# Kernel optimization log

Measured on AMD Instinct MI355X. Metric: run time of the kernel, lower is better.

Reference implementation:

```python
import jax, jax.numpy as jnp
import numpy as np

D_MODEL = 1024
NUM_HEADS = 16
D_K = D_MODEL // NUM_HEADS
NEG = -1000000000.0


def setup_inputs() -> dict:
    key = jax.random.key(0)
    ks = jax.random.split(key, 9)
    B, S, D = 2, 2048, D_MODEL
    scale = 1.0 / np.sqrt(D)
    return {
        "query": jax.random.normal(ks[0], (B, S, D), jnp.float32),
        "key": jax.random.normal(ks[1], (B, S, D), jnp.float32),
        "value": jax.random.normal(ks[2], (B, S, D), jnp.float32),
        "mask": jax.random.randint(ks[3], (B, S, S), 0, 2, jnp.int32),
        # torch nn.Linear stores weight as (out_features, in_features); y = x @ W.T
        "W_q": jax.random.normal(ks[4], (D, D), jnp.float32) * scale,
        "W_k": jax.random.normal(ks[5], (D, D), jnp.float32) * scale,
        "W_v": jax.random.normal(ks[6], (D, D), jnp.float32) * scale,
        "W_o": jax.random.normal(ks[7], (D, D), jnp.float32) * scale,
        "b_o": jax.random.normal(ks[8], (D,), jnp.float32) * 0.01,
    }


def reference(query, key, value, mask, W_q, W_k, W_v, W_o, b_o):
    B, S, D = query.shape
    H, dk = NUM_HEADS, D_K
    # projections (torch Linear: x @ W.T), then split heads -> [B, H, S, dk]
    def split_heads(x, W):
        return jnp.einsum('bsd,ed->bse', x, W).reshape(B, S, H, dk).transpose(0, 2, 1, 3)
    Q = split_heads(query, W_q)
    K = split_heads(key, W_k)
    V = split_heads(value, W_v)
    scores = jnp.einsum('bhqd,bhkd->bhqk', Q, K) / jnp.sqrt(jnp.float32(dk))
    scores = jnp.where(mask[:, None, :, :] == 0, NEG, scores)
    attn = jax.nn.softmax(scores, axis=-1)  # dropout inactive in eval mode
    out = jnp.einsum('bhqk,bhkd->bhqd', attn, V)  # [B, H, S, dk]
    out = out.transpose(0, 2, 1, 3).reshape(B, S, D)
    return jnp.einsum('bsd,ed->bse', out, W_o) + b_o
```

## Files before the change

kernel.cpp:

```cpp
#include <hip/hip_runtime.h>
#include <hip/hip_bf16.h>
#include <stdint.h>

typedef __attribute__((ext_vector_type(4))) float f32x4;
typedef __attribute__((ext_vector_type(8))) short bf16x8;
typedef __attribute__((ext_vector_type(4))) unsigned short us4;
typedef unsigned short ushort_t;
typedef unsigned long long u64;

#define LOG2E 1.44269504088896340f
#define NEGB  -1.0e9f

__device__ __forceinline__ unsigned short f2bf(float x){
  union { float f; uint32_t u; } v; v.f = x;
  uint32_t u = v.u + 0x7fffu + ((v.u >> 16) & 1u);
  return (unsigned short)(u >> 16);
}

__device__ __forceinline__ void gld16(const void* g, void* l){
  __builtin_amdgcn_global_load_lds(
      (const __attribute__((address_space(1))) unsigned int*)g,
      (__attribute__((address_space(3))) unsigned int*)l, 16, 0, 0);
}

__global__ void prep_all(const float4* __restrict__ q, const float4* __restrict__ k,
                         const float4* __restrict__ v, const float4* __restrict__ wq,
                         const float4* __restrict__ wk, const float4* __restrict__ wv,
                         const float4* __restrict__ wo, ushort_t* __restrict__ dst){
  int i = blockIdx.x * 256 + threadIdx.x;
  const float4* src; int base;
  if      (i < 1048576){ src = q;  base = 0; }
  else if (i < 2097152){ src = k;  base = 1048576; }
  else if (i < 3145728){ src = v;  base = 2097152; }
  else if (i < 3407872){ src = wq; base = 3145728; }
  else if (i < 3670016){ src = wk; base = 3407872; }
  else if (i < 3932160){ src = wv; base = 3670016; }
  else                 { src = wo; base = 3932160; }
  float4 f = src[i - base];
  us4 o; o.x = f2bf(f.x); o.y = f2bf(f.y); o.z = f2bf(f.z); o.w = f2bf(f.w);
  ((us4*)dst)[i] = o;
}

__global__ void gemm_qkv(const ushort_t* __restrict__ qb, const ushort_t* __restrict__ kb,
                         const ushort_t* __restrict__ vb, const ushort_t* __restrict__ wqb,
                         const ushort_t* __restrict__ wkb, const ushort_t* __restrict__ wvb,
                         ushort_t* __restrict__ Qh, ushort_t* __restrict__ Kh,
                         ushort_t* __restrict__ Vt, float qscale,
                         const int4* __restrict__ mask, u64* __restrict__ mb){
  __shared__ ushort_t smem[16384];
#define AsQ(c) (smem + (c)*4096)
#define BsQ(c) (smem + 8192 + (c)*4096)
  const int z = blockIdx.z;
  if (z == 3){
    int bid2 = blockIdx.x + (blockIdx.y << 5);
    #pragma unroll
    for (int rep = 0; rep < 2; rep++){
      int w = bid2 * 512 + rep * 256 + threadIdx.x;
      const int4* p = mask + (size_t)w * 16;
      u64 bits = 0;
      #pragma unroll
      for (int j = 0; j < 16; j++){
        int4 m = p[j];
        bits |= (u64)(m.x != 0) << (j*4);
        bits |= (u64)(m.y != 0) << (j*4+1);
        bits |= (u64)(m.z != 0) << (j*4+2);
        bits |= (u64)(m.w != 0) << (j*4+3);
      }
      mb[w] = bits;
    }
    return;
  }
  const ushort_t* A = (z == 0) ? qb  : (z == 1) ? kb  : vb;
  const ushort_t* B = (z == 0) ? wqb : (z == 1) ? wkb : wvb;
  ushort_t*       C = (z == 0) ? Qh  : (z == 1) ? Kh  : Vt;
  const float scale = (z == 0) ? qscale : 1.0f;

  const int tid = threadIdx.x, wave = tid >> 6, lane = tid & 63;
  const int l15 = lane & 15;
  const int m0 = blockIdx.x * 128, n0 = blockIdx.y * 128;
  const int wr = wave >> 1, wc = wave & 1;
  f32x4 acc[4][4] = {};

  const ushort_t* Ag = A + (size_t)(m0 + wave*16 + (lane>>2)) * 1024 + (lane&3)*8;
  const ushort_t* Bg = B + (size_t)(n0 + wave*16 + (lane>>2)) * 1024 + (lane&3)*8;

#define GSTAGE(k0, c) do { \
    gld16(Ag + (k0),         AsQ(c) + wave*512); \
    gld16(Ag + 65536 + (k0), AsQ(c) + (4+wave)*512); \
    gld16(Bg + (k0),         BsQ(c) + wave*512); \
    gld16(Bg + 65536 + (k0), BsQ(c) + (4+wave)*512); } while(0)

  GSTAGE(0, 0);
  int cur = 0;
  for (int k0 = 0; k0 < 1024; k0 += 32){
    __syncthreads();
    if (k0 < 992) GSTAGE(k0 + 32, cur ^ 1);
    bf16x8 a[4], b[4];
    #pragma unroll
    for (int i = 0; i < 4; i++){
      a[i] = *(const bf16x8*)&AsQ(cur)[(wr*64 + i*16 + l15)*32 + (lane>>4)*8];
      b[i] = *(const bf16x8*)&BsQ(cur)[(wc*64 + i*16 + l15)*32 + (lane>>4)*8];
    }
    __builtin_amdgcn_s_setprio(1);
    #pragma unroll
    for (int i = 0; i < 4; i++)
      #pragma unroll
      for (int j = 0; j < 4; j++)
        acc[i][j] = __builtin_amdgcn_mfma_f32_16x16x32_bf16(a[i], b[j], acc[i][j], 0, 0, 0);
    __builtin_amdgcn_s_setprio(0);
    cur ^= 1;
  }

  if (z < 2){
    #pragma unroll
    for (int i = 0; i < 4; i++){
      #pragma unroll
      for (int j = 0; j < 4; j++){
        #pragma unroll
        for (int r = 0; r < 4; r++){
          int row = m0 + wr*64 + i*16 + (lane>>4)*4 + r;
          int col = n0 + wc*64 + j*16 + l15;
          int bb = row >> 11, s = row & 2047, h = col >> 6, d = col & 63;
          C[((size_t)(bb*16 + h)*2048 + s)*64 + d] = f2bf(acc[i][j][r] * scale);
        }
      }
    }
  } else {
    ushort_t* T = smem;
    #pragma unroll
    for (int hh = 0; hh < 2; hh++){
      __syncthreads();
      if (wc == hh){
        #pragma unroll
        for (int i = 0; i < 4; i++){
          #pragma unroll
          for (int j = 0; j < 4; j++){
            int n = j*16 + l15;
            int mb2 = wr*64 + i*16 + (lane>>4)*4;
            us4 pk;
            pk.x = f2bf(acc[i][j][0]); pk.y = f2bf(acc[i][j][1]);
            pk.z = f2bf(acc[i][j][2]); pk.w = f2bf(acc[i][j][3]);
            *(us4*)&T[n*136 + mb2] = pk;
          }
        }
      }
      __syncthreads();
      #pragma unroll
      for (int cc = 0; cc < 4; cc++){
        int chunk = cc*256 + tid;
        int n = chunk >> 4, mc = chunk & 15;
        uint4 val = *(uint4*)&T[n*136 + mc*8];
        int col = n0 + hh*64 + n;
        int hcol = col >> 6, d = col & 63;
        int row = m0 + mc*8;
        int bb2 = row >> 11, s = row & 2047;
        *(uint4*)&C[((size_t)(bb2*16 + hcol)*64 + d)*2048 + s] = val;
      }
    }
  }
}

__global__ void gemm_out(const ushort_t* __restrict__ A, const ushort_t* __restrict__ B,
                         float* __restrict__ C, const float* __restrict__ bias){
  __shared__ ushort_t As[2][4096];
  __shared__ ushort_t Bs[2][4096];
  const int tid = threadIdx.x, wave = tid >> 6, lane = tid & 63;
  const int m0 = blockIdx.x * 128, n0 = blockIdx.y * 128;
  const int wr = wave >> 1, wc = wave & 1;
  f32x4 acc[4][4] = {};

  const ushort_t* Ag = A + (size_t)(m0 + wave*16 + (lane>>2)) * 1024 + (lane&3)*8;
  const ushort_t* Bg = B + (size_t)(n0 + wave*16 + (lane>>2)) * 1024 + (lane&3)*8;

#define GSTAGE2(k0, c) do { \
    gld16(Ag + (k0),         &As[c][wave*512]); \
    gld16(Ag + 65536 + (k0), &As[c][(4+wave)*512]); \
    gld16(Bg + (k0),         &Bs[c][wave*512]); \
    gld16(Bg + 65536 + (k0), &Bs[c][(4+wave)*512]); } while(0)

  GSTAGE2(0, 0);
  int cur = 0;
  for (int k0 = 0; k0 < 1024; k0 += 32){
    __syncthreads();
    if (k0 < 992) GSTAGE2(k0 + 32, cur ^ 1);
    bf16x8 a[4], b[4];
    #pragma unroll
    for (int i = 0; i < 4; i++){
      a[i] = *(const bf16x8*)&As[cur][(wr*64 + i*16 + (lane&15))*32 + (lane>>4)*8];
      b[i] = *(const bf16x8*)&Bs[cur][(wc*64 + i*16 + (lane&15))*32 + (lane>>4)*8];
    }
    __builtin_amdgcn_s_setprio(1);
    #pragma unroll
    for (int i = 0; i < 4; i++)
      #pragma unroll
      for (int j = 0; j < 4; j++)
        acc[i][j] = __builtin_amdgcn_mfma_f32_16x16x32_bf16(a[i], b[j], acc[i][j], 0, 0, 0);
    __builtin_amdgcn_s_setprio(0);
    cur ^= 1;
  }

  #pragma unroll
  for (int i = 0; i < 4; i++){
    #pragma unroll
    for (int j = 0; j < 4; j++){
      #pragma unroll
      for (int r = 0; r < 4; r++){
        int row = m0 + wr*64 + i*16 + (lane>>4)*4 + r;
        int col = n0 + wc*64 + j*16 + (lane&15);
        C[(size_t)row * 1024 + col] = acc[i][j][r] + bias[col];
      }
    }
  }
}

__global__ void attn_fused(const ushort_t* __restrict__ Qh, const ushort_t* __restrict__ Kh,
                           const ushort_t* __restrict__ Vt, const u64* __restrict__ MB,
                           ushort_t* __restrict__ AO){
  __shared__ ushort_t Ks[2][4096];
  __shared__ ushort_t Vs[2][4096];
  __shared__ ushort_t Pb[8][1024];

  const int tid = threadIdx.x, wave = tid >> 6, lane = tid & 63;
  const int g = lane >> 4, l15 = lane & 15;
  const int wg = ((blockIdx.x & 7) << 6) | (blockIdx.x >> 3);
  const int qt = wg & 15, h = (wg >> 4) & 15, b = wg >> 8;
  const int q0 = qt * 128;

  const ushort_t* Qb = Qh + ((size_t)(b*16 + h)*2048 + q0) * 64;
  const ushort_t* Kb = Kh + ((size_t)(b*16 + h)*2048) * 64;
  const ushort_t* Vb = Vt + ((size_t)(b*16 + h)*64) * 2048;
  const u64* wp = MB + ((size_t)b*2048 + q0 + wave*16 + l15) * 32;

  bf16x8 qf[2];
  #pragma unroll
  for (int ks = 0; ks < 2; ks++)
    qf[ks] = *(const bf16x8*)&Qb[(wave*16 + l15)*64 + ks*32 + g*8];

  bf16x8 onesb;
  #pragma unroll
  for (int j = 0; j < 8; j++) onesb[j] = (short)0x3F80;

  f32x4 o[4] = {};
  f32x4 osum = {};

  const int srow = lane >> 3;
  const int scol = ((lane & 7) * 16) ^ (srow << 4);
  const ushort_t* Kg = Kb + (size_t)(wave*8 + srow)*64   + (scol >> 1);
  const ushort_t* Vg = Vb + (size_t)(wave*8 + srow)*2048 + (scol >> 1);
  ushort_t* pb = &Pb[wave][0];
  const int xv = (l15 & 7) << 4;
  const int g4 = g * 4;

#define ASTAGE(t, c) do { \
    gld16(Kg + (size_t)(t)*4096, &Ks[c][wave*512]); \
    gld16(Vg + (t)*64,           &Vs[c][wave*512]); } while(0)

  ASTAGE(0, 0);
  u64 w = wp[0];
  int cur = 0;

  for (int t = 0; t < 32; t++){
    __syncthreads();
    if (t < 31) ASTAGE(t + 1, cur ^ 1);
    u64 wnext = (t < 31) ? wp[t + 1] : 0;

    f32x4 sa[4] = {};
    __builtin_amdgcn_s_setprio(1);
    #pragma unroll
    for (int nf = 0; nf < 4; nf++){
      #pragma unroll
      for (int ks = 0; ks < 2; ks++){
        int row = nf*16 + l15;
        int cb  = (ks*64 + g*16) ^ ((row & 7) << 4);
        bf16x8 kf = *(const bf16x8*)&Ks[cur][row*64 + (cb >> 1)];
        sa[nf] = __builtin_amdgcn_mfma_f32_16x16x32_bf16(kf, qf[ks], sa[nf], 0, 0, 0);
      }
    }
    __builtin_amdgcn_s_setprio(0);

    uint32_t s0 = ((uint32_t)w) >> g4;
    uint32_t s1 = ((uint32_t)(w >> 32)) >> g4;
    float p[4][4];
    #pragma unroll
    for (int nf = 0; nf < 4; nf++){
      uint32_t ws = (nf < 2) ? s0 : s1;
      const int sh = (nf & 1) * 16;
      #pragma unroll
      for (int r = 0; r < 4; r++){
        float s = ((ws >> (sh + r)) & 1u) ? sa[nf][r] : NEGB;
        p[nf][r] = __builtin_amdgcn_exp2f(s);
      }
    }

    #pragma unroll
    for (int nf = 0; nf < 4; nf++){
      __hip_bfloat162 lo, hi;
      lo.x = __float2bfloat16(p[nf][0]); lo.y = __float2bfloat16(p[nf][1]);
      hi.x = __float2bfloat16(p[nf][2]); hi.y = __float2bfloat16(p[nf][3]);
      uint2 pk; pk.x = *(uint32_t*)&lo; pk.y = *(uint32_t*)&hi;
      int byte = l15*128 + ((nf*32 + g*8) ^ xv);
      *(uint2*)((char*)pb + byte) = pk;
    }
    asm volatile("s_waitcnt lgkmcnt(0)" ::: "memory");

    bf16x8 pa[2];
    #pragma unroll
    for (int c = 0; c < 2; c++){
      int cb = (c*64 + g*16) ^ xv;
      pa[c] = *(const bf16x8*)((const char*)pb + l15*128 + cb);
    }
    __builtin_amdgcn_s_setprio(1);
    #pragma unroll
    for (int df = 0; df < 4; df++){
      #pragma unroll
      for (int c = 0; c < 2; c++){
        int vrow = df*16 + l15;
        int cb = (c*64 + g*16) ^ ((vrow & 7) << 4);
        bf16x8 vf = *(const bf16x8*)&Vs[cur][vrow*64 + (cb >> 1)];
        o[df] = __builtin_amdgcn_mfma_f32_16x16x32_bf16(pa[c], vf, o[df], 0, 0, 0);
      }
    }
    osum = __builtin_amdgcn_mfma_f32_16x16x32_bf16(pa[0], onesb, osum, 0, 0, 0);
    osum = __builtin_amdgcn_mfma_f32_16x16x32_bf16(pa[1], onesb, osum, 0, 0, 0);
    __builtin_amdgcn_s_setprio(0);
    w = wnext;
    cur ^= 1;
  }

  float li[4];
  #pragma unroll
  for (int r = 0; r < 4; r++) li[r] = 1.0f / osum[r];
  #pragma unroll
  for (int df = 0; df < 4; df++){
    #pragma unroll
    for (int r = 0; r < 4; r++){
      int s = q0 + wave*16 + g4 + r;
      int d = h*64 + df*16 + l15;
      AO[((size_t)b*2048 + s)*1024 + d] = f2bf(o[df][r] * li[r]);
    }
  }
}

extern "C" void kernel_launch(void* const* d_in, const int* in_sizes, int n_in,
                              void* d_out, int out_size, void* d_ws, size_t ws_size,
                              hipStream_t stream){
  const float* q   = (const float*)d_in[0];
  const float* k   = (const float*)d_in[1];
  const float* v   = (const float*)d_in[2];
  const int*   msk = (const int*)  d_in[3];
  const float* wq  = (const float*)d_in[4];
  const float* wk  = (const float*)d_in[5];
  const float* wv  = (const float*)d_in[6];
  const float* wo  = (const float*)d_in[7];
  const float* bo  = (const float*)d_in[8];

  char* ws = (char*)d_ws;
  ushort_t* conv = (ushort_t*)ws;
  ushort_t* qb  = conv;
  ushort_t* kb  = conv + 4194304;
  ushort_t* vb  = conv + 8388608;
  ushort_t* wqb = conv + 12582912;
  ushort_t* wkb = conv + 13631488;
  ushort_t* wvb = conv + 14680064;
  ushort_t* wob = conv + 15728640;
  u64*      mbits = (u64*)(ws + 33554432);
  ushort_t* Qh  = (ushort_t*)(ws + 34603008);
  ushort_t* Kh  = (ushort_t*)(ws + 42991616);
  ushort_t* Vt  = (ushort_t*)d_out;
  ushort_t* AO  = qb;

  prep_all<<<16384, 256, 0, stream>>>((const float4*)q, (const float4*)k,
      (const float4*)v, (const float4*)wq, (const float4*)wk, (const float4*)wv,
      (const float4*)wo, conv);

  const float qscale = 0.125f * LOG2E;
  gemm_qkv<<<dim3(32, 8, 4), 256, 0, stream>>>(qb, kb, vb, wqb, wkb, wvb,
                                               Qh, Kh, Vt, qscale,
                                               (const int4*)msk, mbits);

  attn_fused<<<512, 512, 0, stream>>>(Qh, Kh, Vt, mbits, AO);

  gemm_out<<<dim3(32, 8), 256, 0, stream>>>(AO, wob, (float*)d_out, bo);
}
```

Baseline: 135.6 us.

## Fuse fp32-to-bf16 activation conversion into QKV projection GEMM loads

The separate conversion pass over the query, key and value activations is removed. The QKV GEMM now loads fp32 activations into registers, packs them to bf16 and writes them to LDS itself, overlapping that work with the MFMA loop, while the weights are still pre-converted by a smaller prep kernel. This avoids writing and re-reading roughly 25MB of bf16 activations. In exchange, each GEMM tile re-reads fp32 activations from global memory (8 column blocks per row block), which doubles the bytes per A load and adds register-staged conversion work inside the loop.

```diff
diff --git a/kernel.cpp b/kernel.cpp
--- a/kernel.cpp
+++ b/kernel.cpp
@@ -17,32 +17,35 @@
   return (unsigned short)(u >> 16);
 }
 
+__device__ __forceinline__ uint32_t pkbf(float a, float b){
+  __hip_bfloat162 t;
+  t.x = __float2bfloat16(a); t.y = __float2bfloat16(b);
+  union { __hip_bfloat162 h; uint32_t u; } c; c.h = t;
+  return c.u;
+}
+
 __device__ __forceinline__ void gld16(const void* g, void* l){
   __builtin_amdgcn_global_load_lds(
       (const __attribute__((address_space(1))) unsigned int*)g,
       (__attribute__((address_space(3))) unsigned int*)l, 16, 0, 0);
 }
 
-__global__ void prep_all(const float4* __restrict__ q, const float4* __restrict__ k,
-                         const float4* __restrict__ v, const float4* __restrict__ wq,
-                         const float4* __restrict__ wk, const float4* __restrict__ wv,
-                         const float4* __restrict__ wo, ushort_t* __restrict__ dst){
+__global__ void prep_w(const float4* __restrict__ wq, const float4* __restrict__ wk,
+                       const float4* __restrict__ wv, const float4* __restrict__ wo,
+                       ushort_t* __restrict__ dst){
   int i = blockIdx.x * 256 + threadIdx.x;
   const float4* src; int base;
-  if      (i < 1048576){ src = q;  base = 0; }
-  else if (i < 2097152){ src = k;  base = 1048576; }
-  else if (i < 3145728){ src = v;  base = 2097152; }
-  else if (i < 3407872){ src = wq; base = 3145728; }
-  else if (i < 3670016){ src = wk; base = 3407872; }
-  else if (i < 3932160){ src = wv; base = 3670016; }
-  else                 { src = wo; base = 3932160; }
+  if      (i < 262144){ src = wq; base = 0; }
+  else if (i < 524288){ src = wk; base = 262144; }
+  else if (i < 786432){ src = wv; base = 524288; }
+  else                { src = wo; base = 786432; }
   float4 f = src[i - base];
   us4 o; o.x = f2bf(f.x); o.y = f2bf(f.y); o.z = f2bf(f.z); o.w = f2bf(f.w);
-  ((us4*)dst)[i] = o;
-}
-
-__global__ void gemm_qkv(const ushort_t* __restrict__ qb, const ushort_t* __restrict__ kb,
-                         const ushort_t* __restrict__ vb, const ushort_t* __restrict__ wqb,
+  ((us4*)dst)[3145728 + i] = o;
+}
+
+__global__ void gemm_qkv(const float* __restrict__ qf32, const float* __restrict__ kf32,
+                         const float* __restrict__ vf32, const ushort_t* __restrict__ wqb,
                          const ushort_t* __restrict__ wkb, const ushort_t* __restrict__ wvb,
                          ushort_t* __restrict__ Qh, ushort_t* __restrict__ Kh,
                          ushort_t* __restrict__ Vt, float qscale,
@@ -70,9 +73,9 @@
     }
     return;
   }
-  const ushort_t* A = (z == 0) ? qb  : (z == 1) ? kb  : vb;
-  const ushort_t* B = (z == 0) ? wqb : (z == 1) ? wkb : wvb;
-  ushort_t*       C = (z == 0) ? Qh  : (z == 1) ? Kh  : Vt;
+  const float*    A = (z == 0) ? qf32 : (z == 1) ? kf32 : vf32;
+  const ushort_t* B = (z == 0) ? wqb  : (z == 1) ? wkb  : wvb;
+  ushort_t*       C = (z == 0) ? Qh   : (z == 1) ? Kh   : Vt;
   const float scale = (z == 0) ? qscale : 1.0f;
 
   const int tid = threadIdx.x, wave = tid >> 6, lane = tid & 63;
@@ -81,20 +84,33 @@
   const int wr = wave >> 1, wc = wave & 1;
   f32x4 acc[4][4] = {};
 
-  const ushort_t* Ag = A + (size_t)(m0 + wave*16 + (lane>>2)) * 1024 + (lane&3)*8;
+  const float*    Ag = A + (size_t)(m0 + wave*16 + (lane>>2)) * 1024 + (lane&3)*8;
   const ushort_t* Bg = B + (size_t)(n0 + wave*16 + (lane>>2)) * 1024 + (lane&3)*8;
 
-#define GSTAGE(k0, c) do { \
-    gld16(Ag + (k0),         AsQ(c) + wave*512); \
-    gld16(Ag + 65536 + (k0), AsQ(c) + (4+wave)*512); \
+#define WSTAGE(k0, c) do { \
     gld16(Bg + (k0),         BsQ(c) + wave*512); \
     gld16(Bg + 65536 + (k0), BsQ(c) + (4+wave)*512); } while(0)
 
-  GSTAGE(0, 0);
+  float4 ar[4];
+#define ALOAD(k0) do { \
+    ar[0] = *(const float4*)(Ag + (k0)); \
+    ar[1] = *(const float4*)(Ag + (k0) + 4); \
+    ar[2] = *(const float4*)(Ag + 65536 + (k0)); \
+    ar[3] = *(const float4*)(Ag + 65536 + (k0) + 4); } while(0)
+#define AWRITE(c) do { \
+    uint4 w0, w1; \
+    w0.x = pkbf(ar[0].x, ar[0].y); w0.y = pkbf(ar[0].z, ar[0].w); \
+    w0.z = pkbf(ar[1].x, ar[1].y); w0.w = pkbf(ar[1].z, ar[1].w); \
+    w1.x = pkbf(ar[2].x, ar[2].y); w1.y = pkbf(ar[2].z, ar[2].w); \
+    w1.z = pkbf(ar[3].x, ar[3].y); w1.w = pkbf(ar[3].z, ar[3].w); \
+    *(uint4*)(AsQ(c) + wave*512 + lane*8)     = w0; \
+    *(uint4*)(AsQ(c) + (4+wave)*512 + lane*8) = w1; } while(0)
+
+  ALOAD(0); WSTAGE(0, 0); AWRITE(0);
   int cur = 0;
   for (int k0 = 0; k0 < 1024; k0 += 32){
     __syncthreads();
-    if (k0 < 992) GSTAGE(k0 + 32, cur ^ 1);
+    if (k0 < 992){ ALOAD(k0 + 32); WSTAGE(k0 + 32, cur ^ 1); }
     bf16x8 a[4], b[4];
     #pragma unroll
     for (int i = 0; i < 4; i++){
@@ -108,6 +124,7 @@
       for (int j = 0; j < 4; j++)
         acc[i][j] = __builtin_amdgcn_mfma_f32_16x16x32_bf16(a[i], b[j], acc[i][j], 0, 0, 0);
     __builtin_amdgcn_s_setprio(0);
+    if (k0 < 992) AWRITE(cur ^ 1);
     cur ^= 1;
   }
 
@@ -356,9 +373,6 @@
 
   char* ws = (char*)d_ws;
   ushort_t* conv = (ushort_t*)ws;
-  ushort_t* qb  = conv;
-  ushort_t* kb  = conv + 4194304;
-  ushort_t* vb  = conv + 8388608;
   ushort_t* wqb = conv + 12582912;
   ushort_t* wkb = conv + 13631488;
   ushort_t* wvb = conv + 14680064;
@@ -367,14 +381,13 @@
   ushort_t* Qh  = (ushort_t*)(ws + 34603008);
   ushort_t* Kh  = (ushort_t*)(ws + 42991616);
   ushort_t* Vt  = (ushort_t*)d_out;
-  ushort_t* AO  = qb;
-
-  prep_all<<<16384, 256, 0, stream>>>((const float4*)q, (const float4*)k,
-      (const float4*)v, (const float4*)wq, (const float4*)wk, (const float4*)wv,
-      (const float4*)wo, conv);
+  ushort_t* AO  = conv;
+
+  prep_w<<<4096, 256, 0, stream>>>((const float4*)wq, (const float4*)wk,
+                                   (const float4*)wv, (const float4*)wo, conv);
 
   const float qscale = 0.125f * LOG2E;
-  gemm_qkv<<<dim3(32, 8, 4), 256, 0, stream>>>(qb, kb, vb, wqb, wkb, wvb,
+  gemm_qkv<<<dim3(32, 8, 4), 256, 0, stream>>>(q, k, v, wqb, wkb, wvb,
                                                Qh, Kh, Vt, qscale,
                                                (const int4*)msk, mbits);
 
```

Measured after the change: 226.0 us. 1.67x slower.
